# Kernel optimization log

Measured on AMD Instinct MI355X. Metric: run time of the kernel, lower is better.

## Reference

```python
import jax, jax.numpy as jnp
import numpy as np

B, S, IN_DIM, D_MODEL, H = 1, 4096, 512, 512, 8
DK = D_MODEL // H


def setup_inputs() -> dict:
    key = jax.random.key(0)
    ks = jax.random.split(key, 10)
    sc_in = 1.0 / np.sqrt(IN_DIM)
    sc_dm = 1.0 / np.sqrt(D_MODEL)
    return {
        "x": jax.random.normal(ks[0], (B, S, IN_DIM), dtype=jnp.float32),
        "mask": jax.random.randint(ks[1], (1, 1, S, S), 0, 2, dtype=jnp.int32),
        "wq_w": jax.random.uniform(ks[2], (D_MODEL, IN_DIM), jnp.float32, -sc_in, sc_in),
        "wq_b": jax.random.uniform(ks[3], (D_MODEL,), jnp.float32, -sc_in, sc_in),
        "wk_w": jax.random.uniform(ks[4], (D_MODEL, IN_DIM), jnp.float32, -sc_in, sc_in),
        "wk_b": jax.random.uniform(ks[5], (D_MODEL,), jnp.float32, -sc_in, sc_in),
        "wv_w": jax.random.uniform(ks[6], (D_MODEL, IN_DIM), jnp.float32, -sc_in, sc_in),
        "wv_b": jax.random.uniform(ks[7], (D_MODEL,), jnp.float32, -sc_in, sc_in),
        "dense_w": jax.random.uniform(ks[8], (D_MODEL, D_MODEL), jnp.float32, -sc_dm, sc_dm),
        "dense_b": jax.random.uniform(ks[9], (D_MODEL,), jnp.float32, -sc_dm, sc_dm),
    }


def _split_heads(t):
    # Faithful to original: raw view [B, S, D] -> [B, H, S, DK] (no transpose)
    return t.reshape(B, H, S, DK)


def reference(x, mask, wq_w, wq_b, wk_w, wk_b, wv_w, wv_b, dense_w, dense_b):
    q = _split_heads(x @ wq_w.T + wq_b)  # [B, H, S, DK]
    k = _split_heads(x @ wk_w.T + wk_b)
    v = _split_heads(x @ wv_w.T + wv_b)
    score = jnp.einsum("bhqd,bhkd->bhqk", q, k) / np.sqrt(DK).astype(np.float32)
    score = score + mask.astype(score.dtype) * (-1e9)
    attn = jax.nn.softmax(score, axis=-1)
    out = jnp.einsum("bhqk,bhkd->bhqd", attn, v)  # [B, H, S, DK]
    out = out.transpose(0, 2, 1, 3).reshape(B, S, D_MODEL)
    return out @ dense_w.T + dense_b
```

## Files before the change

kernel.cpp:

```cpp
#include <hip/hip_runtime.h>
#include <hip/hip_bf16.h>

#define S_LEN 4096
#define DM    512
#define NH    8
#define DK    64

typedef __attribute__((ext_vector_type(8))) __bf16 bf16x8;
typedef __attribute__((ext_vector_type(4))) float  f32x4;
typedef unsigned short u16;
typedef unsigned int   u32;
typedef unsigned long long u64;

#define SQ_SCALE (0.125f * 1.44269504f)
#define FMAX 12.0f

#define NPART 4
#define KSPAN 1024

__device__ __forceinline__ u16 f2bf(float f) {
  union { float f; u32 i; } v; v.f = f;
  u32 r = v.i + 0x7fff + ((v.i >> 16) & 1);
  return (u16)(r >> 16);
}
__device__ __forceinline__ float bf2f(u16 u) {
  union { u32 i; float f; } v; v.i = ((u32)u) << 16; return v.f;
}

__device__ __forceinline__ void gl_lds16(const u16* g, u16* l) {
  __builtin_amdgcn_global_load_lds(
      (const __attribute__((address_space(1))) u32*)g,
      (__attribute__((address_space(3))) u32*)l, 16, 0, 0);
}

__global__ __launch_bounds__(256) void pack_mask(const int* __restrict__ mask,
                                                 u64* __restrict__ out) {
  int gid = blockIdx.x * 256 + threadIdx.x;
  u64 b = __ballot(mask[gid] != 0);
  if ((threadIdx.x & 63) == 0) out[gid >> 6] = b;
}

__global__ __launch_bounds__(256) void convert_all(
    const float* __restrict__ x, const float* __restrict__ wq,
    const float* __restrict__ wk, const float* __restrict__ wv,
    const float* __restrict__ dw,
    u16* __restrict__ xb, u16* __restrict__ wcat, u16* __restrict__ dwb) {
  int b = blockIdx.x;
  const float* src; u16* dst; size_t off;
  if      (b < 2048) { src = x;  dst = xb;   off = (size_t)b * 1024; }
  else if (b < 2304) { src = wq; dst = wcat; off = (size_t)(b - 2048) * 1024; }
  else if (b < 2560) { src = wk; dst = wcat + 262144; off = (size_t)(b - 2304) * 1024; }
  else if (b < 2816) { src = wv; dst = wcat + 524288; off = (size_t)(b - 2560) * 1024; }
  else               { src = dw; dst = dwb;  off = (size_t)(b - 2816) * 1024; }
  size_t i = off + (size_t)threadIdx.x * 4;
  float4 v = *reinterpret_cast<const float4*>(src + i);
  ushort4 o = make_ushort4(f2bf(v.x), f2bf(v.y), f2bf(v.z), f2bf(v.w));
  *reinterpret_cast<ushort4*>(dst + i) = o;
}

__global__ __launch_bounds__(256) void qkv_gemm(
    const u16* __restrict__ A, const u16* __restrict__ Wcat,
    const float* __restrict__ bq, const float* __restrict__ bk,
    const float* __restrict__ bv,
    u16* __restrict__ Qb, u16* __restrict__ Kb, u16* __restrict__ V4) {
  __shared__ u16 As[2][64 * 64];
  __shared__ u16 Ws[2][128 * 64];
  const int t = threadIdx.x;
  const int lane = t & 63, wv = t >> 6;
  const int m16 = lane & 15, quad = lane >> 4;
  const int n0g = blockIdx.x * 128, m0 = blockIdx.y * 64;
  const int seg = n0g >> 9;
  const int n0 = n0g & 511;
  const int mq = wv >> 1, nq = wv & 1;

  const u16* asrc[2]; int ldsoA[2];
#pragma unroll
  for (int c0 = 0; c0 < 2; c0++) {
    int c = t + c0 * 256;
    int row = c >> 3, swc = ((c & 7) ^ (row & 7)) * 8;
    asrc[c0] = A + (size_t)(m0 + row) * DM + swc;
    ldsoA[c0] = c * 8;
  }
  const u16* wsrc[4]; int ldsoW[4];
#pragma unroll
  for (int c0 = 0; c0 < 4; c0++) {
    int c = t + c0 * 256;
    int row = c >> 3, swc = ((c & 7) ^ (row & 7)) * 8;
    wsrc[c0] = Wcat + (size_t)(n0g + row) * DM + swc;
    ldsoW[c0] = c * 8;
  }

  f32x4 acc[2][4];
#pragma unroll
  for (int i = 0; i < 2; i++)
#pragma unroll
    for (int j = 0; j < 4; j++) acc[i][j] = (f32x4)0.f;

#pragma unroll
  for (int c0 = 0; c0 < 2; c0++) gl_lds16(asrc[c0], &As[0][ldsoA[c0]]);
#pragma unroll
  for (int c0 = 0; c0 < 4; c0++) gl_lds16(wsrc[c0], &Ws[0][ldsoW[c0]]);
  __syncthreads();

  const int xorv = m16 & 7;
  int cur = 0;
  for (int k0 = 0; k0 < DM; k0 += 64) {
    if (k0 + 64 < DM) {
#pragma unroll
      for (int c0 = 0; c0 < 2; c0++)
        gl_lds16(asrc[c0] + k0 + 64, &As[cur ^ 1][ldsoA[c0]]);
#pragma unroll
      for (int c0 = 0; c0 < 4; c0++)
        gl_lds16(wsrc[c0] + k0 + 64, &Ws[cur ^ 1][ldsoW[c0]]);
    }
    const u16* Ac = As[cur];
    const u16* Wc = Ws[cur];
#pragma unroll
    for (int kk = 0; kk < 64; kk += 32) {
      const int gcol = (((quad + (kk >> 3)) ^ xorv) * 8);
      bf16x8 a0 = *reinterpret_cast<const bf16x8*>(&Ac[(mq * 32 + m16) * 64 + gcol]);
      bf16x8 a1 = *reinterpret_cast<const bf16x8*>(&Ac[(mq * 32 + 16 + m16) * 64 + gcol]);
#pragma unroll
      for (int ct = 0; ct < 4; ct++) {
        bf16x8 b = *reinterpret_cast<const bf16x8*>(&Wc[(nq * 64 + ct * 16 + m16) * 64 + gcol]);
        acc[0][ct] = __builtin_amdgcn_mfma_f32_16x16x32_bf16(a0, b, acc[0][ct], 0, 0, 0);
        acc[1][ct] = __builtin_amdgcn_mfma_f32_16x16x32_bf16(a1, b, acc[1][ct], 0, 0, 0);
      }
    }
    __syncthreads();
    cur ^= 1;
  }

  const float* bias = (seg == 0) ? bq : (seg == 1) ? bk : bv;
  const float scale = (seg == 0) ? SQ_SCALE : 1.f;
  float bn[4];
#pragma unroll
  for (int ct = 0; ct < 4; ct++) bn[ct] = bias[n0 + nq * 64 + ct * 16 + m16];

  if (seg == 2) {
    u16* T = &Ws[0][0];
#pragma unroll
    for (int rt = 0; rt < 2; rt++)
#pragma unroll
      for (int ct = 0; ct < 4; ct++)
#pragma unroll
        for (int r = 0; r < 4; r++)
          T[(nq * 64 + ct * 16 + m16) * 72 + mq * 32 + rt * 16 + quad * 4 + r] =
              f2bf(acc[rt][ct][r] + bn[ct]);
    __syncthreads();
    const int h    = m0 >> 9;
    const int mp   = m0 & 511;
    const int cseg = n0 >> 7;
#pragma unroll
    for (int c0 = 0; c0 < 4; c0++) {
      int c = t + c0 * 256;
      int d  = c >> 4;
      int tl = (c >> 1) & 7;
      int cl = c & 1;
      uint4 v = *reinterpret_cast<const uint4*>(&T[(cl * 64 + d) * 72 + tl * 8]);
      *reinterpret_cast<uint4*>(
          &V4[(size_t)(h * 64 + d) * 4096 + ((mp >> 3) + tl) * 64 + cl * 32 + cseg * 8]) = v;
    }
  } else {
    u16* dst = (seg == 0) ? Qb : Kb;
#pragma unroll
    for (int rt = 0; rt < 2; rt++)
#pragma unroll
      for (int ct = 0; ct < 4; ct++) {
        int n = n0 + nq * 64 + ct * 16 + m16;
#pragma unroll
        for (int r = 0; r < 4; r++) {
          int m = m0 + mq * 32 + rt * 16 + quad * 4 + r;
          dst[(size_t)m * DM + n] = f2bf((acc[rt][ct][r] + bn[ct]) * scale);
        }
      }
  }
}

__global__ __launch_bounds__(256) void dense_gemm(
    const u16* __restrict__ A, const u16* __restrict__ W,
    const float* __restrict__ bias, float* __restrict__ Cout) {
  __shared__ u16 As[2][64 * 64];
  __shared__ u16 Ws[2][64 * 64];
  const int t = threadIdx.x;
  const int lane = t & 63, wv = t >> 6;
  const int m16 = lane & 15, quad = lane >> 4;
  const int n0 = blockIdx.x * 64, m0 = blockIdx.y * 64;

  const u16* asrc[2]; const u16* wsrc[2]; int ldso[2];
#pragma unroll
  for (int c0 = 0; c0 < 2; c0++) {
    int c = t + c0 * 256;
    int row = c >> 3, swc = ((c & 7) ^ (row & 7)) * 8;
    asrc[c0] = A + (size_t)(m0 + row) * DM + swc;
    wsrc[c0] = W + (size_t)(n0 + row) * DM + swc;
    ldso[c0] = c * 8;
  }

  f32x4 acc[4];
#pragma unroll
  for (int j = 0; j < 4; j++) acc[j] = (f32x4)0.f;

#pragma unroll
  for (int c0 = 0; c0 < 2; c0++) {
    gl_lds16(asrc[c0], &As[0][ldso[c0]]);
    gl_lds16(wsrc[c0], &Ws[0][ldso[c0]]);
  }
  __syncthreads();

  const int xorv = m16 & 7;
  int cur = 0;
  for (int k0 = 0; k0 < DM; k0 += 64) {
    if (k0 + 64 < DM) {
#pragma unroll
      for (int c0 = 0; c0 < 2; c0++) {
        gl_lds16(asrc[c0] + k0 + 64, &As[cur ^ 1][ldso[c0]]);
        gl_lds16(wsrc[c0] + k0 + 64, &Ws[cur ^ 1][ldso[c0]]);
      }
    }
    const u16* Ac = As[cur];
    const u16* Wc = Ws[cur];
#pragma unroll
    for (int kk = 0; kk < 64; kk += 32) {
      const int gcol = (((quad + (kk >> 3)) ^ xorv) * 8);
      bf16x8 a = *reinterpret_cast<const bf16x8*>(&Ac[(wv * 16 + m16) * 64 + gcol]);
#pragma unroll
      for (int ct = 0; ct < 4; ct++) {
        bf16x8 b = *reinterpret_cast<const bf16x8*>(&Wc[(ct * 16 + m16) * 64 + gcol]);
        acc[ct] = __builtin_amdgcn_mfma_f32_16x16x32_bf16(a, b, acc[ct], 0, 0, 0);
      }
    }
    __syncthreads();
    cur ^= 1;
  }

  float bn[4];
#pragma unroll
  for (int ct = 0; ct < 4; ct++) bn[ct] = bias[n0 + ct * 16 + m16];
#pragma unroll
  for (int ct = 0; ct < 4; ct++) {
    int n = n0 + ct * 16 + m16;
#pragma unroll
    for (int r = 0; r < 4; r++) {
      int m = m0 + wv * 16 + quad * 4 + r;
      Cout[(size_t)m * DM + n] = acc[ct][r] + bn[ct];
    }
  }
}

__device__ __forceinline__ void pack_p(const f32x4* s, u32 lo, u32 hi,
                                       uint4& o0, uint4& o1) {
  u32 pk[8];
#pragma unroll
  for (int ct = 0; ct < 4; ct++) {
    u32 w = (ct & 1) ? hi : lo;
    int b = ct >> 1;
    float p0 = __builtin_amdgcn_exp2f(((w >> b) & 1u)        ? -1e9f : s[ct][0]);
    float p1 = __builtin_amdgcn_exp2f(((w >> (b + 8)) & 1u)  ? -1e9f : s[ct][1]);
    float p2 = __builtin_amdgcn_exp2f(((w >> (b + 16)) & 1u) ? -1e9f : s[ct][2]);
    float p3 = __builtin_amdgcn_exp2f(((w >> (b + 24)) & 1u) ? -1e9f : s[ct][3]);
    pk[2 * ct]     = __builtin_amdgcn_perm(__float_as_uint(p1) + 0x8000u,
                                           __float_as_uint(p0) + 0x8000u, 0x07060302u);
    pk[2 * ct + 1] = __builtin_amdgcn_perm(__float_as_uint(p3) + 0x8000u,
                                           __float_as_uint(p2) + 0x8000u, 0x07060302u);
  }
  o0 = make_uint4(pk[0], pk[1], pk[2], pk[3]);
  o1 = make_uint4(pk[4], pk[5], pk[6], pk[7]);
}

__global__ __launch_bounds__(256, 4) void attn_mfma(
    const u16* __restrict__ Q, const u16* __restrict__ K,
    const u16* __restrict__ V4, const u64* __restrict__ mbits,
    u16* __restrict__ Op, float* __restrict__ Lp) {
  __shared__ u16 Ks[2][64 * 64];
  __shared__ u16 Vs[2][64 * 64];

  const int t = threadIdx.x;
  const int lane = t & 63, w4 = t >> 6;
  const int m16 = lane & 15, quad = lane >> 4;
  const int lin = blockIdx.x;
  const int q0 = ((lin >> 3) & 31) * 128;
  const int hg = ((lin >> 8) << 3) | (lin & 7);
  const int h = hg & 7;
  const int g = hg >> 3;
  const size_t hoff = (size_t)h * S_LEN * DK;
  const size_t kbase = hoff + (size_t)g * KSPAN * DK;

  const u16* qpA = Q + hoff + (size_t)(q0 + w4 * 32 + m16) * DK + quad * 8;
  bf16x8 qloA = *reinterpret_cast<const bf16x8*>(qpA);
  bf16x8 qhiA = *reinterpret_cast<const bf16x8*>(qpA + 32);
  bf16x8 qloB = *reinterpret_cast<const bf16x8*>(qpA + 16 * DK);
  bf16x8 qhiB = *reinterpret_cast<const bf16x8*>(qpA + 16 * DK + 32);

  union { u16 u[8]; bf16x8 v; } onesu;
#pragma unroll
  for (int j = 0; j < 8; j++) onesu.u[j] = 0x3F80;
  const bf16x8 ones = onesu.v;

  const int l = lane;
  const int colu = ((l & 7) ^ (l >> 3)) * 8;
  const u16* kp[2]; const u16* vp[2]; int ldso[2];
#pragma unroll
  for (int i = 0; i < 2; i++) {
    int row = (w4 * 2 + i) * 8 + (l >> 3);
    int inv = (((row >> 4) & 1) << 5) | (((row >> 1) & 1) << 4) | ((row & 1) << 3) |
              (((row >> 3) & 1) << 2) | (((row >> 2) & 1) << 1) | ((row >> 5) & 1);
    kp[i] = K + kbase + (size_t)inv * DK + colu;
    vp[i] = V4 + (size_t)(h * 64 + row) * 4096 + g * KSPAN + colu;
    ldso[i] = (w4 * 2 + i) * 512 + l * 8;
  }

  const u64* mpA = &mbits[(size_t)(q0 + w4 * 32 + m16) * 64 + ((g * KSPAN) >> 6)];
  const u64* mpB = mpA + (size_t)16 * 64;

  f32x4 accA[4], accB[4];
  f32x4 acc_lA = (f32x4)0.f, acc_lB = (f32x4)0.f;
#pragma unroll
  for (int dt = 0; dt < 4; dt++) { accA[dt] = (f32x4)0.f; accB[dt] = (f32x4)0.f; }

#pragma unroll
  for (int i = 0; i < 2; i++) {
    gl_lds16(kp[i], &Ks[0][ldso[i]]);
    gl_lds16(vp[i], &Vs[0][ldso[i]]);
  }
  u64 rmA = mpA[0], rmB = mpB[0];
  __syncthreads();

  const int xorv = (m16 & 7) * 8;
  int cur = 0;
#pragma unroll 1
  for (int k0 = 0; k0 < KSPAN; k0 += 64) {
    if (k0 + 64 < KSPAN) {
#pragma unroll
      for (int i = 0; i < 2; i++) {
        gl_lds16(kp[i] + (size_t)(k0 + 64) * DK, &Ks[cur ^ 1][ldso[i]]);
        gl_lds16(vp[i] + (k0 + 64),              &Vs[cur ^ 1][ldso[i]]);
      }
    }
    u64 mqA = rmA >> (2 * quad);
    u64 mqB = rmB >> (2 * quad);
    if (k0 + 64 < KSPAN) { rmA = mpA[(k0 >> 6) + 1]; rmB = mpB[(k0 >> 6) + 1]; }

    const u16* Kc = Ks[cur];
    const u16* Vc = Vs[cur];

    f32x4 sA[4], sB[4];
#pragma unroll
    for (int ct = 0; ct < 4; ct++) { sA[ct] = (f32x4)(-FMAX); sB[ct] = (f32x4)(-FMAX); }
#pragma unroll
    for (int ct = 0; ct < 4; ct++) {
      const int rb = (ct * 16 + m16) * 64;
      bf16x8 klo = *reinterpret_cast<const bf16x8*>(&Kc[rb + ((quad * 8) ^ xorv)]);
      bf16x8 khi = *reinterpret_cast<const bf16x8*>(&Kc[rb + ((quad * 8 + 32) ^ xorv)]);
      sA[ct] = __builtin_amdgcn_mfma_f32_16x16x32_bf16(klo, qloA, sA[ct], 0, 0, 0);
      sA[ct] = __builtin_amdgcn_mfma_f32_16x16x32_bf16(khi, qhiA, sA[ct], 0, 0, 0);
      sB[ct] = __builtin_amdgcn_mfma_f32_16x16x32_bf16(klo, qloB, sB[ct], 0, 0, 0);
      sB[ct] = __builtin_amdgcn_mfma_f32_16x16x32_bf16(khi, qhiB, sB[ct], 0, 0, 0);
    }

    union { uint4 i; bf16x8 v; } pA0, pA1, pB0, pB1;
    pack_p(sA, (u32)mqA, (u32)(mqA >> 32), pA0.i, pA1.i);
    pack_p(sB, (u32)mqB, (u32)(mqB >> 32), pB0.i, pB1.i);

#pragma unroll
    for (int dt = 0; dt < 4; dt++) {
      const int rb = (dt * 16 + m16) * 64;
      bf16x8 vlo = *reinterpret_cast<const bf16x8*>(&Vc[rb + ((quad * 8) ^ xorv)]);
      bf16x8 vhi = *reinterpret_cast<const bf16x8*>(&Vc[rb + ((quad * 8 + 32) ^ xorv)]);
      accA[dt] = __builtin_amdgcn_mfma_f32_16x16x32_bf16(pA0.v, vlo, accA[dt], 0, 0, 0);
      accA[dt] = __builtin_amdgcn_mfma_f32_16x16x32_bf16(pA1.v, vhi, accA[dt], 0, 0, 0);
      accB[dt] = __builtin_amdgcn_mfma_f32_16x16x32_bf16(pB0.v, vlo, accB[dt], 0, 0, 0);
      accB[dt] = __builtin_amdgcn_mfma_f32_16x16x32_bf16(pB1.v, vhi, accB[dt], 0, 0, 0);
    }
    acc_lA = __builtin_amdgcn_mfma_f32_16x16x32_bf16(pA0.v, ones, acc_lA, 0, 0, 0);
    acc_lA = __builtin_amdgcn_mfma_f32_16x16x32_bf16(pA1.v, ones, acc_lA, 0, 0, 0);
    acc_lB = __builtin_amdgcn_mfma_f32_16x16x32_bf16(pB0.v, ones, acc_lB, 0, 0, 0);
    acc_lB = __builtin_amdgcn_mfma_f32_16x16x32_bf16(pB1.v, ones, acc_lB, 0, 0, 0);

    __syncthreads();
    cur ^= 1;
  }

  u16* Og = Op + (size_t)g * 2097152;
#pragma unroll
  for (int dt = 0; dt < 4; dt++)
#pragma unroll
    for (int r = 0; r < 4; r++) {
      Og[(size_t)(q0 + w4 * 32 + quad * 4 + r) * DM + h * DK + dt * 16 + m16] =
          f2bf(accA[dt][r]);
      Og[(size_t)(q0 + w4 * 32 + 16 + quad * 4 + r) * DM + h * DK + dt * 16 + m16] =
          f2bf(accB[dt][r]);
    }
  if (m16 == 0) {
#pragma unroll
    for (int r = 0; r < 4; r++) {
      Lp[g * 32768 + h * 4096 + q0 + w4 * 32 + quad * 4 + r] = acc_lA[r];
      Lp[g * 32768 + h * 4096 + q0 + w4 * 32 + 16 + quad * 4 + r] = acc_lB[r];
    }
  }
}

__global__ __launch_bounds__(256) void attn_merge(
    const u16* __restrict__ Op, const float* __restrict__ Lp,
    u16* __restrict__ Out) {
  int i8 = (blockIdx.x * 256 + threadIdx.x) * 8;
  int q = i8 >> 9;
  int h = (i8 >> 6) & 7;
  float l = 0.f;
#pragma unroll
  for (int part = 0; part < NPART; part++) l += Lp[part * 32768 + h * 4096 + q];
  float rl = 1.f / l;
  float o[8];
#pragma unroll
  for (int j = 0; j < 8; j++) o[j] = 0.f;
#pragma unroll
  for (int part = 0; part < NPART; part++) {
    ushort4 v0 = *reinterpret_cast<const ushort4*>(Op + (size_t)part * 2097152 + i8);
    ushort4 v1 = *reinterpret_cast<const ushort4*>(Op + (size_t)part * 2097152 + i8 + 4);
    o[0] += bf2f(v0.x); o[1] += bf2f(v0.y); o[2] += bf2f(v0.z); o[3] += bf2f(v0.w);
    o[4] += bf2f(v1.x); o[5] += bf2f(v1.y); o[6] += bf2f(v1.z); o[7] += bf2f(v1.w);
  }
  ushort4 o0 = make_ushort4(f2bf(o[0] * rl), f2bf(o[1] * rl),
                            f2bf(o[2] * rl), f2bf(o[3] * rl));
  ushort4 o1 = make_ushort4(f2bf(o[4] * rl), f2bf(o[5] * rl),
                            f2bf(o[6] * rl), f2bf(o[7] * rl));
  *reinterpret_cast<ushort4*>(Out + i8) = o0;
  *reinterpret_cast<ushort4*>(Out + i8 + 4) = o1;
}

extern "C" void kernel_launch(void* const* d_in, const int* in_sizes, int n_in,
                              void* d_out, int out_size, void* d_ws, size_t ws_size,
                              hipStream_t stream) {
  const float* x    = (const float*)d_in[0];
  const int*   mask = (const int*)d_in[1];
  const float* wq_w = (const float*)d_in[2];
  const float* wq_b = (const float*)d_in[3];
  const float* wk_w = (const float*)d_in[4];
  const float* wk_b = (const float*)d_in[5];
  const float* wv_w = (const float*)d_in[6];
  const float* wv_b = (const float*)d_in[7];
  const float* dw   = (const float*)d_in[8];
  const float* db   = (const float*)d_in[9];

  u16* xb    = (u16*)d_ws;
  u16* wcat  = xb    + 2097152;
  u16* dwb   = wcat  + 786432;
  u16* Qb    = dwb   + 262144;
  u16* Kb    = Qb    + 2097152;
  u16* V4    = Kb    + 2097152;
  u16* Opart = V4    + 2097152;
  u64* mb    = (u64*)(Opart + (size_t)NPART * 2097152);
  float* Lp  = (float*)(mb + 262144);

  pack_mask<<<(S_LEN * S_LEN) / 256, 256, 0, stream>>>(mask, mb);
  convert_all<<<3072, 256, 0, stream>>>(x, wq_w, wk_w, wv_w, dw, xb, wcat, dwb);

  qkv_gemm<<<dim3(12, 64), 256, 0, stream>>>(xb, wcat, wq_b, wk_b, wv_b,
                                             Qb, Kb, V4);

  attn_mfma<<<1024, 256, 0, stream>>>(Qb, Kb, V4, mb, Opart, Lp);
  attn_merge<<<1024, 256, 0, stream>>>(Opart, Lp, Qb);

  dense_gemm<<<dim3(8, 64), 256, 0, stream>>>(Qb, dwb, db, (float*)d_out);
}
```

Baseline: 219.7 us.

## Fuse prep kernels, fold mask into score init, merge split-K in last block

```diff
diff --git a/kernel.cpp b/kernel.cpp
--- a/kernel.cpp
+++ b/kernel.cpp
@@ -27,35 +27,49 @@
   union { u32 i; float f; } v; v.i = ((u32)u) << 16; return v.f;
 }
 
+__device__ __forceinline__ u32 cvtpk(float a, float b) {
+  u32 r;
+  asm("v_cvt_pk_bf16_f32 %0, %1, %2" : "=v"(r) : "v"(a), "v"(b));
+  return r;
+}
+
 __device__ __forceinline__ void gl_lds16(const u16* g, u16* l) {
   __builtin_amdgcn_global_load_lds(
       (const __attribute__((address_space(1))) u32*)g,
       (__attribute__((address_space(3))) u32*)l, 16, 0, 0);
 }
 
-__global__ __launch_bounds__(256) void pack_mask(const int* __restrict__ mask,
-                                                 u64* __restrict__ out) {
-  int gid = blockIdx.x * 256 + threadIdx.x;
-  u64 b = __ballot(mask[gid] != 0);
-  if ((threadIdx.x & 63) == 0) out[gid >> 6] = b;
-}
-
-__global__ __launch_bounds__(256) void convert_all(
-    const float* __restrict__ x, const float* __restrict__ wq,
-    const float* __restrict__ wk, const float* __restrict__ wv,
-    const float* __restrict__ dw,
-    u16* __restrict__ xb, u16* __restrict__ wcat, u16* __restrict__ dwb) {
-  int b = blockIdx.x;
-  const float* src; u16* dst; size_t off;
-  if      (b < 2048) { src = x;  dst = xb;   off = (size_t)b * 1024; }
-  else if (b < 2304) { src = wq; dst = wcat; off = (size_t)(b - 2048) * 1024; }
-  else if (b < 2560) { src = wk; dst = wcat + 262144; off = (size_t)(b - 2304) * 1024; }
-  else if (b < 2816) { src = wv; dst = wcat + 524288; off = (size_t)(b - 2560) * 1024; }
-  else               { src = dw; dst = dwb;  off = (size_t)(b - 2816) * 1024; }
-  size_t i = off + (size_t)threadIdx.x * 4;
-  float4 v = *reinterpret_cast<const float4*>(src + i);
-  ushort4 o = make_ushort4(f2bf(v.x), f2bf(v.y), f2bf(v.z), f2bf(v.w));
-  *reinterpret_cast<ushort4*>(dst + i) = o;
+__global__ __launch_bounds__(256) void prep(
+    const int* __restrict__ mask, const float* __restrict__ x,
+    const float* __restrict__ wq, const float* __restrict__ wk,
+    const float* __restrict__ wv, const float* __restrict__ dw,
+    u64* __restrict__ mb, u16* __restrict__ xb, u16* __restrict__ wcat,
+    u16* __restrict__ dwb, int* __restrict__ ctr) {
+  const int b = blockIdx.x, t = threadIdx.x;
+  if (b < 16384) {
+    const int lane = t & 63, w4 = t >> 6;
+    const int wb = b * 16 + w4 * 4;
+    u64 b0 = __ballot(mask[(size_t)(wb + 0) * 64 + lane] != 0);
+    u64 b1 = __ballot(mask[(size_t)(wb + 1) * 64 + lane] != 0);
+    u64 b2 = __ballot(mask[(size_t)(wb + 2) * 64 + lane] != 0);
+    u64 b3 = __ballot(mask[(size_t)(wb + 3) * 64 + lane] != 0);
+    if (lane == 0) {
+      mb[wb] = b0; mb[wb + 1] = b1; mb[wb + 2] = b2; mb[wb + 3] = b3;
+    }
+    if (b == 0) ctr[t] = 0;
+  } else {
+    const int c = b - 16384;
+    const float* src; u16* dst; size_t off;
+    if      (c < 2048) { src = x;  dst = xb;   off = (size_t)c * 1024; }
+    else if (c < 2304) { src = wq; dst = wcat; off = (size_t)(c - 2048) * 1024; }
+    else if (c < 2560) { src = wk; dst = wcat + 262144; off = (size_t)(c - 2304) * 1024; }
+    else if (c < 2816) { src = wv; dst = wcat + 524288; off = (size_t)(c - 2560) * 1024; }
+    else               { src = dw; dst = dwb;  off = (size_t)(c - 2816) * 1024; }
+    size_t i = off + (size_t)t * 4;
+    float4 v = *reinterpret_cast<const float4*>(src + i);
+    ushort4 o = make_ushort4(f2bf(v.x), f2bf(v.y), f2bf(v.z), f2bf(v.w));
+    *reinterpret_cast<ushort4*>(dst + i) = o;
+  }
 }
 
 __global__ __launch_bounds__(256) void qkv_gemm(
@@ -248,21 +262,16 @@
   }
 }
 
-__device__ __forceinline__ void pack_p(const f32x4* s, u32 lo, u32 hi,
-                                       uint4& o0, uint4& o1) {
+__device__ __forceinline__ void pack_p(const f32x4* s, uint4& o0, uint4& o1) {
   u32 pk[8];
 #pragma unroll
   for (int ct = 0; ct < 4; ct++) {
-    u32 w = (ct & 1) ? hi : lo;
-    int b = ct >> 1;
-    float p0 = __builtin_amdgcn_exp2f(((w >> b) & 1u)        ? -1e9f : s[ct][0]);
-    float p1 = __builtin_amdgcn_exp2f(((w >> (b + 8)) & 1u)  ? -1e9f : s[ct][1]);
-    float p2 = __builtin_amdgcn_exp2f(((w >> (b + 16)) & 1u) ? -1e9f : s[ct][2]);
-    float p3 = __builtin_amdgcn_exp2f(((w >> (b + 24)) & 1u) ? -1e9f : s[ct][3]);
-    pk[2 * ct]     = __builtin_amdgcn_perm(__float_as_uint(p1) + 0x8000u,
-                                           __float_as_uint(p0) + 0x8000u, 0x07060302u);
-    pk[2 * ct + 1] = __builtin_amdgcn_perm(__float_as_uint(p3) + 0x8000u,
-                                           __float_as_uint(p2) + 0x8000u, 0x07060302u);
+    float p0 = __builtin_amdgcn_exp2f(s[ct][0]);
+    float p1 = __builtin_amdgcn_exp2f(s[ct][1]);
+    float p2 = __builtin_amdgcn_exp2f(s[ct][2]);
+    float p3 = __builtin_amdgcn_exp2f(s[ct][3]);
+    pk[2 * ct]     = cvtpk(p0, p1);
+    pk[2 * ct + 1] = cvtpk(p2, p3);
   }
   o0 = make_uint4(pk[0], pk[1], pk[2], pk[3]);
   o1 = make_uint4(pk[4], pk[5], pk[6], pk[7]);
@@ -271,9 +280,11 @@
 __global__ __launch_bounds__(256, 4) void attn_mfma(
     const u16* __restrict__ Q, const u16* __restrict__ K,
     const u16* __restrict__ V4, const u64* __restrict__ mbits,
-    u16* __restrict__ Op, float* __restrict__ Lp) {
+    u16* __restrict__ Op, float* __restrict__ Lp,
+    u16* __restrict__ Ob, int* __restrict__ ctr) {
   __shared__ u16 Ks[2][64 * 64];
   __shared__ u16 Vs[2][64 * 64];
+  __shared__ int last;
 
   const int t = threadIdx.x;
   const int lane = t & 63, w4 = t >> 6;
@@ -345,8 +356,20 @@
     const u16* Vc = Vs[cur];
 
     f32x4 sA[4], sB[4];
-#pragma unroll
-    for (int ct = 0; ct < 4; ct++) { sA[ct] = (f32x4)(-FMAX); sB[ct] = (f32x4)(-FMAX); }
+    u32 loA = (u32)mqA, hiA = (u32)(mqA >> 32);
+    u32 loB = (u32)mqB, hiB = (u32)(mqB >> 32);
+#pragma unroll
+    for (int ct = 0; ct < 4; ct++) {
+      u32 wA = (ct & 1) ? hiA : loA;
+      u32 wB = (ct & 1) ? hiB : loB;
+      int b = ct >> 1;
+#pragma unroll
+      for (int r = 0; r < 4; r++) {
+        sA[ct][r] = ((wA >> (b + 8 * r)) & 1u) ? -1e9f : -FMAX;
+        sB[ct][r] = ((wB >> (b + 8 * r)) & 1u) ? -1e9f : -FMAX;
+      }
+    }
+
 #pragma unroll
     for (int ct = 0; ct < 4; ct++) {
       const int rb = (ct * 16 + m16) * 64;
@@ -359,8 +382,8 @@
     }
 
     union { uint4 i; bf16x8 v; } pA0, pA1, pB0, pB1;
-    pack_p(sA, (u32)mqA, (u32)(mqA >> 32), pA0.i, pA1.i);
-    pack_p(sB, (u32)mqB, (u32)(mqB >> 32), pB0.i, pB1.i);
+    pack_p(sA, pA0.i, pA1.i);
+    pack_p(sB, pB0.i, pB1.i);
 
 #pragma unroll
     for (int dt = 0; dt < 4; dt++) {
@@ -398,34 +421,39 @@
       Lp[g * 32768 + h * 4096 + q0 + w4 * 32 + 16 + quad * 4 + r] = acc_lB[r];
     }
   }
-}
-
-__global__ __launch_bounds__(256) void attn_merge(
-    const u16* __restrict__ Op, const float* __restrict__ Lp,
-    u16* __restrict__ Out) {
-  int i8 = (blockIdx.x * 256 + threadIdx.x) * 8;
-  int q = i8 >> 9;
-  int h = (i8 >> 6) & 7;
-  float l = 0.f;
-#pragma unroll
-  for (int part = 0; part < NPART; part++) l += Lp[part * 32768 + h * 4096 + q];
-  float rl = 1.f / l;
-  float o[8];
-#pragma unroll
-  for (int j = 0; j < 8; j++) o[j] = 0.f;
-#pragma unroll
-  for (int part = 0; part < NPART; part++) {
-    ushort4 v0 = *reinterpret_cast<const ushort4*>(Op + (size_t)part * 2097152 + i8);
-    ushort4 v1 = *reinterpret_cast<const ushort4*>(Op + (size_t)part * 2097152 + i8 + 4);
-    o[0] += bf2f(v0.x); o[1] += bf2f(v0.y); o[2] += bf2f(v0.z); o[3] += bf2f(v0.w);
-    o[4] += bf2f(v1.x); o[5] += bf2f(v1.y); o[6] += bf2f(v1.z); o[7] += bf2f(v1.w);
-  }
-  ushort4 o0 = make_ushort4(f2bf(o[0] * rl), f2bf(o[1] * rl),
-                            f2bf(o[2] * rl), f2bf(o[3] * rl));
-  ushort4 o1 = make_ushort4(f2bf(o[4] * rl), f2bf(o[5] * rl),
-                            f2bf(o[6] * rl), f2bf(o[7] * rl));
-  *reinterpret_cast<ushort4*>(Out + i8) = o0;
-  *reinterpret_cast<ushort4*>(Out + i8 + 4) = o1;
+
+  __threadfence();
+  if (t == 0) last = atomicAdd(&ctr[(q0 >> 7) * 8 + h], 1);
+  __syncthreads();
+  if (last == 3) {
+#pragma unroll
+    for (int jj = 0; jj < 4; jj++) {
+      int ch = t * 4 + jj;
+      int ql = ch >> 3, d0 = (ch & 7) * 8;
+      int q = q0 + ql;
+      float ls = Lp[h * 4096 + q] + Lp[32768 + h * 4096 + q] +
+                 Lp[65536 + h * 4096 + q] + Lp[98304 + h * 4096 + q];
+      float rl = 1.f / ls;
+      float o[8];
+#pragma unroll
+      for (int j = 0; j < 8; j++) o[j] = 0.f;
+#pragma unroll
+      for (int p = 0; p < NPART; p++) {
+        const u16* src = Op + (size_t)p * 2097152 + (size_t)q * DM + h * DK + d0;
+        ushort4 v0 = *reinterpret_cast<const ushort4*>(src);
+        ushort4 v1 = *reinterpret_cast<const ushort4*>(src + 4);
+        o[0] += bf2f(v0.x); o[1] += bf2f(v0.y); o[2] += bf2f(v0.z); o[3] += bf2f(v0.w);
+        o[4] += bf2f(v1.x); o[5] += bf2f(v1.y); o[6] += bf2f(v1.z); o[7] += bf2f(v1.w);
+      }
+      ushort4 o0 = make_ushort4(f2bf(o[0] * rl), f2bf(o[1] * rl),
+                                f2bf(o[2] * rl), f2bf(o[3] * rl));
+      ushort4 o1 = make_ushort4(f2bf(o[4] * rl), f2bf(o[5] * rl),
+                                f2bf(o[6] * rl), f2bf(o[7] * rl));
+      u16* dst = Ob + (size_t)q * DM + h * DK + d0;
+      *reinterpret_cast<ushort4*>(dst) = o0;
+      *reinterpret_cast<ushort4*>(dst + 4) = o1;
+    }
+  }
 }
 
 extern "C" void kernel_launch(void* const* d_in, const int* in_sizes, int n_in,
@@ -449,17 +477,18 @@
   u16* Kb    = Qb    + 2097152;
   u16* V4    = Kb    + 2097152;
   u16* Opart = V4    + 2097152;
-  u64* mb    = (u64*)(Opart + (size_t)NPART * 2097152);
+  u16* Ob    = Opart + (size_t)NPART * 2097152;
+  u64* mb    = (u64*)(Ob + 2097152);
   float* Lp  = (float*)(mb + 262144);
-
-  pack_mask<<<(S_LEN * S_LEN) / 256, 256, 0, stream>>>(mask, mb);
-  convert_all<<<3072, 256, 0, stream>>>(x, wq_w, wk_w, wv_w, dw, xb, wcat, dwb);
+  int* ctr   = (int*)(Lp + 131072);
+
+  prep<<<16384 + 3072, 256, 0, stream>>>(mask, x, wq_w, wk_w, wv_w, dw,
+                                         mb, xb, wcat, dwb, ctr);
 
   qkv_gemm<<<dim3(12, 64), 256, 0, stream>>>(xb, wcat, wq_b, wk_b, wv_b,
                                              Qb, Kb, V4);
 
-  attn_mfma<<<1024, 256, 0, stream>>>(Qb, Kb, V4, mb, Opart, Lp);
-  attn_merge<<<1024, 256, 0, stream>>>(Opart, Lp, Qb);
-
-  dense_gemm<<<dim3(8, 64), 256, 0, stream>>>(Qb, dwb, db, (float*)d_out);
-}
+  attn_mfma<<<1024, 256, 0, stream>>>(Qb, Kb, V4, mb, Opart, Lp, Ob, ctr);
+
+  dense_gemm<<<dim3(8, 64), 256, 0, stream>>>(Ob, dwb, db, (float*)d_out);
+}
```

New measurement: 306.9 us. +39.7%, slower.
